# Performance work log

Hardware: AMD Instinct MI355X
Metric: run time of the kernel (lower is better)

Reference implementation:

```python
import jax, jax.numpy as jnp
import numpy as np

N_NODES = 50000
N_EDGES = 800000
D = 128


def gin_layer(x, edge_index, edge_attr, ee1, ee2, W1, b1, W2, b2):
    # PyG default flow source_to_target: x_j = x[edge_index[0]], aggregate at edge_index[1]
    src, dst = edge_index[0], edge_index[1]
    edge_emb = ee1[edge_attr[:, 0]] + ee2[edge_attr[:, 1]]           # [E, D]
    msg = x[src] + edge_emb                                          # [E, D]
    aggr = jax.ops.segment_sum(msg, dst, num_segments=x.shape[0])    # [N, D]
    h = jax.nn.relu(aggr @ W1 + b1)                                  # [N, 2D]
    return h @ W2 + b2                                               # [N, out]


def setup_inputs() -> dict:
    key = jax.random.key(0)
    ks = jax.random.split(key, 16)
    s = 1.0 / np.sqrt(D)
    inp = {
        "x": jax.random.normal(ks[0], (N_NODES, D), jnp.float32),
        "edge_index": jax.random.randint(ks[1], (2, N_EDGES), 0, N_NODES, dtype=jnp.int32),
        "edge_attr": jax.random.randint(ks[2], (N_EDGES, 2), 0, 3, dtype=jnp.int32),
        "ee1_0": jax.random.normal(ks[3], (6, D), jnp.float32) * s,
        "ee2_0": jax.random.normal(ks[4], (3, D), jnp.float32) * s,
        "W1_0": jax.random.normal(ks[5], (D, 2 * D), jnp.float32) * s,
        "b1_0": jnp.zeros((2 * D,), jnp.float32),
        "W2_0": jax.random.normal(ks[6], (2 * D, D), jnp.float32) * s,
        "b2_0": jnp.zeros((D,), jnp.float32),
        "ee1_1": jax.random.normal(ks[7], (6, D), jnp.float32) * s,
        "ee2_1": jax.random.normal(ks[8], (3, D), jnp.float32) * s,
        "W1_1": jax.random.normal(ks[9], (D, 2 * D), jnp.float32) * s,
        "b1_1": jnp.zeros((2 * D,), jnp.float32),
        "W2_1": jax.random.normal(ks[10], (2 * D, D), jnp.float32) * s,
        "b2_1": jnp.zeros((D,), jnp.float32),
    }
    return inp


def reference(x, edge_index, edge_attr, ee1_0, ee2_0, W1_0, b1_0, W2_0, b2_0,
              ee1_1, ee2_1, W1_1, b1_1, W2_1, b2_1):
    h = gin_layer(x, edge_index, edge_attr, ee1_0, ee2_0, W1_0, b1_0, W2_0, b2_0)
    h = jax.nn.relu(h)  # activation between GNN layers
    out = gin_layer(h, edge_index, edge_attr, ee1_1, ee2_1, W1_1, b1_1, W2_1, b2_1)
    return out  # jk='last'
```

## Files before the change

### kernel.cpp

```cpp
#include <hip/hip_runtime.h>

typedef __attribute__((ext_vector_type(8))) short s16x8;
typedef __attribute__((ext_vector_type(4))) float f32x4;
typedef unsigned short u16;
typedef unsigned char u8;
typedef unsigned long long u64;

#define D_FEAT 128
#define TILE1 4096

__device__ __forceinline__ u16 f2bf(float f) {
    unsigned u = __builtin_bit_cast(unsigned, f);
    u = u + 0x7fffu + ((u >> 16) & 1u);
    return (u16)(u >> 16);
}

__global__ __launch_bounds__(256) void tobf16_kernel(const float4* __restrict__ X,
                                                     u16* __restrict__ out, int n4) {
    int i = blockIdx.x * 256 + threadIdx.x;
    if (i < n4) {
        float4 v = X[i];
        uint2 p;
        p.x = (unsigned)f2bf(v.x) | ((unsigned)f2bf(v.y) << 16);
        p.y = (unsigned)f2bf(v.z) | ((unsigned)f2bf(v.w) << 16);
        *(uint2*)(out + (size_t)i * 4) = p;
    }
}

__global__ __launch_bounds__(256) void hist1_kernel(const int* __restrict__ dst,
                                                    int* __restrict__ ghist,
                                                    int E, int nb1, int bins) {
    __shared__ int h[256];
    const int t = threadIdx.x;
    h[t] = 0;
    __syncthreads();
    const int base = blockIdx.x * TILE1;
    #pragma unroll
    for (int j = 0; j < TILE1 / 256; ++j) {
        int e = base + j * 256 + t;
        if (e < E) atomicAdd(&h[dst[e] >> 8], 1);
    }
    __syncthreads();
    if (t < bins) ghist[t * nb1 + blockIdx.x] = h[t];
}

__global__ __launch_bounds__(256) void scan1a_kernel(int* __restrict__ ghist,
                                                     int* __restrict__ btot, int nb1) {
    __shared__ int wt[4];
    const int t = threadIdx.x, lane = t & 63, wid = t >> 6;
    const int bin = blockIdx.x;
    const int v = (t < nb1) ? ghist[bin * nb1 + t] : 0;
    int s = v;
    #pragma unroll
    for (int off = 1; off < 64; off <<= 1) {
        int u = __shfl_up(s, off, 64);
        if (lane >= off) s += u;
    }
    if (lane == 63) wt[wid] = s;
    __syncthreads();
    int add = 0;
    #pragma unroll
    for (int w = 0; w < 4; ++w) add += (w < wid) ? wt[w] : 0;
    s += add;
    if (t < nb1) ghist[bin * nb1 + t] = s - v;
    if (t == 255) btot[bin] = s;
}

__global__ __launch_bounds__(256) void scan1b_kernel(const int* __restrict__ btot,
                                                     int* __restrict__ bbase,
                                                     int* __restrict__ row_start, int bins) {
    __shared__ int wt[4];
    const int t = threadIdx.x, lane = t & 63, wid = t >> 6;
    const int v = (t < bins) ? btot[t] : 0;
    int s = v;
    #pragma unroll
    for (int off = 1; off < 64; off <<= 1) {
        int u = __shfl_up(s, off, 64);
        if (lane >= off) s += u;
    }
    if (lane == 63) wt[wid] = s;
    __syncthreads();
    int add = 0;
    #pragma unroll
    for (int w = 0; w < 4; ++w) add += (w < wid) ? wt[w] : 0;
    s += add;
    if (t < bins) bbase[t] = s - v;
    if (t == 255) bbase[bins] = s;
    if (t == 0) row_start[0] = 0;
}

__global__ __launch_bounds__(256) void scatter1_kernel(const int* __restrict__ src,
                                                       const int* __restrict__ dst,
                                                       const int* __restrict__ eattr,
                                                       const int* __restrict__ ghist,
                                                       const int* __restrict__ bbase,
                                                       u64* __restrict__ buf1,
                                                       int E, int nb1, int bins) {
    __shared__ int lofs[256];
    const int t = threadIdx.x;
    if (t < bins) lofs[t] = bbase[t] + ghist[t * nb1 + blockIdx.x];
    __syncthreads();
    const int base = blockIdx.x * TILE1;
    #pragma unroll
    for (int j = 0; j < TILE1 / 256; ++j) {
        int e = base + j * 256 + t;
        if (e < E) {
            int d = dst[e];
            int2 at = ((const int2*)eattr)[e];
            unsigned pay = (unsigned)src[e] | ((unsigned)(at.x * 3 + at.y) << 16);
            int pos = atomicAdd(&lofs[d >> 8], 1);
            buf1[pos] = ((u64)(unsigned)d << 32) | pay;
        }
    }
}

__global__ __launch_bounds__(256) void bucket2_kernel(const u64* __restrict__ buf1,
                                                      const int* __restrict__ bbase,
                                                      int* __restrict__ row_start,
                                                      unsigned* __restrict__ edges, int N) {
    __shared__ int cnt[256];
    __shared__ int cur[256];
    __shared__ int wt[4];
    const int t = threadIdx.x, lane = t & 63, wid = t >> 6;
    const int bin = blockIdx.x;
    const int lo = bbase[bin], hi = bbase[bin + 1];
    cnt[t] = 0;
    __syncthreads();
    for (int i = lo + t; i < hi; i += 256)
        atomicAdd(&cnt[(int)(buf1[i] >> 32) & 255], 1);
    __syncthreads();
    const int v = cnt[t];
    int s = v;
    #pragma unroll
    for (int off = 1; off < 64; off <<= 1) {
        int u = __shfl_up(s, off, 64);
        if (lane >= off) s += u;
    }
    if (lane == 63) wt[wid] = s;
    __syncthreads();
    int add = 0;
    #pragma unroll
    for (int w = 0; w < 4; ++w) add += (w < wid) ? wt[w] : 0;
    const int incl = s + add;
    const int g = bin * 256 + t;
    if (g < N) row_start[g + 1] = lo + incl;
    cur[t] = incl - v;
    __syncthreads();
    for (int i = lo + t; i < hi; i += 256) {
        u64 rec = buf1[i];
        int loc = atomicAdd(&cur[(int)(rec >> 32) & 255], 1);
        edges[lo + loc] = (unsigned)rec;
    }
}

__global__ __launch_bounds__(256) void transpose_kernel(const float* __restrict__ W1_0,
                                                        const float* __restrict__ W2_0,
                                                        const float* __restrict__ W1_1,
                                                        const float* __restrict__ W2_1,
                                                        u16* __restrict__ out) {
    int mat = blockIdx.y;
    const float* s = (mat == 0) ? W1_0 : (mat == 1) ? W2_0 : (mat == 2) ? W1_1 : W2_1;
    int K = (mat & 1) ? 256 : 128;
    int Nc = 384 - K;
    u16* d = out + mat * 32768;
    int idx = blockIdx.x * 256 + threadIdx.x;
    int n = idx / K, k = idx - n * K;
    d[idx] = f2bf(s[k * Nc + n]);
}

__global__ __launch_bounds__(128) void emb_kernel(const float* __restrict__ ee1_0,
                                                  const float* __restrict__ ee2_0,
                                                  const float* __restrict__ ee1_1,
                                                  const float* __restrict__ ee2_1,
                                                  float* __restrict__ emb) {
    int code = blockIdx.x;
    int layer = blockIdx.y;
    int d = threadIdx.x;
    int a0 = code / 3, a1 = code - a0 * 3;
    const float* e1 = layer ? ee1_1 : ee1_0;
    const float* e2 = layer ? ee2_1 : ee2_0;
    emb[layer * 18 * 128 + code * 128 + d] = e1[a0 * 128 + d] + e2[a1 * 128 + d];
}

__global__ __launch_bounds__(256) void aggregate_kernel(const u16* __restrict__ X,
                                                        const int* __restrict__ row_start,
                                                        const unsigned* __restrict__ edges,
                                                        const float* __restrict__ emb,
                                                        u16* __restrict__ A, int N) {
    __shared__ float semb[18 * 128];
    for (int i = threadIdx.x; i < 18 * 128; i += 256) semb[i] = emb[i];
    __syncthreads();
    const int node = blockIdx.x * 4 + (threadIdx.x >> 6);
    const int lane = threadIdx.x & 63;
    if (node >= N) return;
    int s = __builtin_amdgcn_readfirstlane(row_start[node]);
    const int e = __builtin_amdgcn_readfirstlane(row_start[node + 1]);
    const float2* sem2 = (const float2*)semb;
    float a0 = 0.f, a1 = 0.f;

    while (s < e) {
        const int take = (e - s < 64) ? (e - s) : 64;
        unsigned pl = edges[s + (lane < take ? lane : 0)];
        #pragma unroll
        for (int c = 0; c < 4; ++c) {
            const int cb = c * 16;
            if (cb < take) {
                unsigned ps[16];
                unsigned xv[16];
                float2 ev[16];
                #pragma unroll
                for (int j = 0; j < 16; ++j)
                    ps[j] = __builtin_amdgcn_readlane(pl, cb + j);
                #pragma unroll
                for (int j = 0; j < 16; ++j)
                    xv[j] = *(const unsigned*)(X + (ps[j] & 0xFFFFu) * D_FEAT + lane * 2);
                #pragma unroll
                for (int j = 0; j < 16; ++j)
                    ev[j] = sem2[(int)(ps[j] >> 16) * 64 + lane];
                #pragma unroll
                for (int j = 0; j < 16; ++j) {
                    const float m = (cb + j < take) ? 1.f : 0.f;
                    a0 += m * (__builtin_bit_cast(float, xv[j] << 16) + ev[j].x);
                    a1 += m * (__builtin_bit_cast(float, xv[j] & 0xFFFF0000u) + ev[j].y);
                }
            }
        }
        s += take;
    }
    unsigned outp = (unsigned)f2bf(a0) | ((unsigned)f2bf(a1) << 16);
    *(unsigned*)(A + node * D_FEAT + lane * 2) = outp;
}

#define HPAD 264
template <bool RELU2, bool OUTF32>
__global__ __launch_bounds__(256, 1) void mlp_kernel(const u16* __restrict__ A,
                                                     const u16* __restrict__ B1t,
                                                     const float* __restrict__ bias1,
                                                     const u16* __restrict__ B2t,
                                                     const float* __restrict__ bias2,
                                                     void* __restrict__ C, int M) {
    __shared__ __align__(16) u16 wbuf[32768];
    __shared__ __align__(16) u16 hh[4][16][HPAD];
    const int tid = threadIdx.x;
    const int wave = tid >> 6;
    const int lane = tid & 63;
    const int m16 = lane & 15;
    const int quad = lane >> 4;

    const int row0 = blockIdx.x * 64 + wave * 16;
    const int arow = row0 + m16;
    const bool avalid = arow < M;

    {
        const uint4* src = (const uint4*)B1t;
        #pragma unroll
        for (int i = 0; i < 16; ++i) {
            int s = i * 256 + tid;
            uint4 v = src[s];
            int c = (((s >> 8) * 4 + ((s >> 2) & 3)) << 6) | ((s & 3) << 4) | ((s >> 4) & 15);
            *(uint4*)(wbuf + c * 8) = v;
        }
    }

    s16x8 af[4];
    #pragma unroll
    for (int kb = 0; kb < 4; ++kb) af[kb] = s16x8{};
    if (avalid) {
        #pragma unroll
        for (int kb = 0; kb < 4; ++kb)
            af[kb] = *(const s16x8*)(A + arow * 128 + kb * 32 + quad * 8);
    }
    float b1v[16];
    #pragma unroll
    for (int t = 0; t < 16; ++t) b1v[t] = bias1[t * 16 + m16];

    __syncthreads();

    f32x4 acc[16];
    #pragma unroll
    for (int t = 0; t < 16; ++t) acc[t] = f32x4{0, 0, 0, 0};

    #pragma unroll
    for (int kb = 0; kb < 4; ++kb) {
        #pragma unroll
        for (int t = 0; t < 16; ++t) {
            s16x8 bf = *(const s16x8*)(wbuf + (((((t << 2) | kb) << 6) | lane) * 8));
            acc[t] = __builtin_amdgcn_mfma_f32_16x16x32_bf16(af[kb], bf, acc[t], 0, 0, 0);
        }
    }

    #pragma unroll
    for (int t = 0; t < 16; ++t) {
        const int col = t * 16 + m16;
        #pragma unroll
        for (int r = 0; r < 4; ++r) {
            float v = acc[t][r] + b1v[t];
            v = v > 0.f ? v : 0.f;
            hh[wave][quad * 4 + r][col] = f2bf(v);
        }
    }
    __syncthreads();

    {
        const uint4* src = (const uint4*)B2t;
        #pragma unroll
        for (int i = 0; i < 16; ++i) {
            int s = i * 256 + tid;
            uint4 v = src[s];
            int c = (((s >> 9) * 8 + ((s >> 2) & 7)) << 6) | ((s & 3) << 4) | ((s >> 5) & 15);
            *(uint4*)(wbuf + c * 8) = v;
        }
    }
    float b2v[8];
    #pragma unroll
    for (int t = 0; t < 8; ++t) b2v[t] = bias2[t * 16 + m16];

    __syncthreads();

    f32x4 acc2[8];
    #pragma unroll
    for (int t = 0; t < 8; ++t) acc2[t] = f32x4{0, 0, 0, 0};

    #pragma unroll
    for (int kb = 0; kb < 8; ++kb) {
        s16x8 haf = *(const s16x8*)(&hh[wave][m16][kb * 32 + quad * 8]);
        #pragma unroll
        for (int t = 0; t < 8; ++t) {
            s16x8 bf = *(const s16x8*)(wbuf + (((((t << 3) | kb) << 6) | lane) * 8));
            acc2[t] = __builtin_amdgcn_mfma_f32_16x16x32_bf16(haf, bf, acc2[t], 0, 0, 0);
        }
    }

    #pragma unroll
    for (int t = 0; t < 8; ++t) {
        const int col = t * 16 + m16;
        #pragma unroll
        for (int r = 0; r < 4; ++r) {
            const int row = row0 + quad * 4 + r;
            if (row < M) {
                float v = acc2[t][r] + b2v[t];
                if (RELU2) v = v > 0.f ? v : 0.f;
                if (OUTF32) ((float*)C)[row * 128 + col] = v;
                else        ((u16*)C)[row * 128 + col] = f2bf(v);
            }
        }
    }
}

extern "C" void kernel_launch(void* const* d_in, const int* in_sizes, int n_in,
                              void* d_out, int out_size, void* d_ws, size_t ws_size,
                              hipStream_t stream) {
    const int N = in_sizes[0] / D_FEAT;
    const int E = in_sizes[1] / 2;

    const float* x    = (const float*)d_in[0];
    const int* eidx   = (const int*)d_in[1];
    const int* eattr  = (const int*)d_in[2];
    const float* ee1_0 = (const float*)d_in[3];
    const float* ee2_0 = (const float*)d_in[4];
    const float* W1_0  = (const float*)d_in[5];
    const float* b1_0  = (const float*)d_in[6];
    const float* W2_0  = (const float*)d_in[7];
    const float* b2_0  = (const float*)d_in[8];
    const float* ee1_1 = (const float*)d_in[9];
    const float* ee2_1 = (const float*)d_in[10];
    const float* W1_1  = (const float*)d_in[11];
    const float* b1_1  = (const float*)d_in[12];
    const float* W2_1  = (const float*)d_in[13];
    const float* b2_1  = (const float*)d_in[14];

    const int nb1  = (E + TILE1 - 1) / TILE1;
    const int bins = (N + 255) / 256;

    char* ws = (char*)d_ws;
    size_t off = 0;
    auto alloc = [&](size_t bytes) { size_t o = off; off = (off + bytes + 255) & ~(size_t)255; return o; };
    size_t o_rowstart = alloc((size_t)(N + 1) * 4);
    size_t o_edges    = alloc((size_t)E * 4);
    size_t o_ghist    = alloc((size_t)bins * nb1 * 4);
    size_t o_base     = alloc((size_t)(bins + 1) * 4);
    size_t o_btot     = alloc((size_t)bins * 4);
    size_t o_emb      = alloc(2 * 18 * 128 * 4);
    size_t o_wt       = alloc(4 * 32768 * 2);
    size_t o_aa       = alloc((size_t)N * D_FEAT * 2);

    int*      row_start = (int*)(ws + o_rowstart);
    unsigned* edges     = (unsigned*)(ws + o_edges);
    int*      ghist     = (int*)(ws + o_ghist);
    int*      bbase     = (int*)(ws + o_base);
    int*      btot      = (int*)(ws + o_btot);
    float*    emb       = (float*)(ws + o_emb);
    u16*      W1t_0     = (u16*)(ws + o_wt);
    u16*      W2t_0     = W1t_0 + 32768;
    u16*      W1t_1     = W2t_0 + 32768;
    u16*      W2t_1     = W1t_1 + 32768;
    u16*      AA        = (u16*)(ws + o_aa);
    u64*      buf1      = (u64*)(ws + o_aa);

    u16* X2 = (u16*)d_out;
    u16* xb = (u16*)d_out + (size_t)N * D_FEAT;

    const int rows64 = (N + 63) / 64;
    const int aggB = (N + 3) / 4;
    const int n4 = N * D_FEAT / 4;

    tobf16_kernel<<<(n4 + 255) / 256, 256, 0, stream>>>((const float4*)x, xb, n4);

    hist1_kernel<<<nb1, 256, 0, stream>>>(eidx + E, ghist, E, nb1, bins);
    scan1a_kernel<<<bins, 256, 0, stream>>>(ghist, btot, nb1);
    scan1b_kernel<<<1, 256, 0, stream>>>(btot, bbase, row_start, bins);
    scatter1_kernel<<<nb1, 256, 0, stream>>>(eidx, eidx + E, eattr, ghist, bbase, buf1, E, nb1, bins);
    bucket2_kernel<<<bins, 256, 0, stream>>>(buf1, bbase, row_start, edges, N);

    emb_kernel<<<dim3(18, 2), 128, 0, stream>>>(ee1_0, ee2_0, ee1_1, ee2_1, emb);
    transpose_kernel<<<dim3(128, 4), 256, 0, stream>>>(W1_0, W2_0, W1_1, W2_1, W1t_0);

    aggregate_kernel<<<aggB, 256, 0, stream>>>(xb, row_start, edges, emb, AA, N);
    mlp_kernel<true, false><<<rows64, 256, 0, stream>>>(AA, W1t_0, b1_0, W2t_0, b2_0, X2, N);

    aggregate_kernel<<<aggB, 256, 0, stream>>>(X2, row_start, edges, emb + 18 * 128, AA, N);
    mlp_kernel<false, true><<<rows64, 256, 0, stream>>>(AA, W1t_1, b1_1, W2t_1, b2_1, d_out, N);
}
```

Before: 305.9 us.

## Make MLP kernel persistent with resident weights, swizzled LDS, and full-chunk aggregate path

The MLP kernel becomes persistent: 256 blocks each load both weight matrices into LDS once (160KB dynamic shared memory) and loop over row tiles, prefetching the next A tile while the current one computes. The hidden buffer uses an XOR swizzle instead of padding to avoid LDS bank conflicts. The aggregate kernel gains a fast path for full 16-edge chunks that skips the per-edge masking multiply. The aim is to stop reloading weights for every 64-row tile. The trade-offs are one block per CU with large LDS, fewer waves to hide latency, and an extra barrier per tile.

```diff
diff --git a/kernel.cpp b/kernel.cpp
--- a/kernel.cpp
+++ b/kernel.cpp
@@ -204,7 +204,25 @@
         #pragma unroll
         for (int c = 0; c < 4; ++c) {
             const int cb = c * 16;
-            if (cb < take) {
+            if (cb + 16 <= take) {
+                unsigned ps[16];
+                unsigned xv[16];
+                float2 ev[16];
+                #pragma unroll
+                for (int j = 0; j < 16; ++j)
+                    ps[j] = __builtin_amdgcn_readlane(pl, cb + j);
+                #pragma unroll
+                for (int j = 0; j < 16; ++j)
+                    xv[j] = *(const unsigned*)(X + (ps[j] & 0xFFFFu) * D_FEAT + lane * 2);
+                #pragma unroll
+                for (int j = 0; j < 16; ++j)
+                    ev[j] = sem2[(int)(ps[j] >> 16) * 64 + lane];
+                #pragma unroll
+                for (int j = 0; j < 16; ++j) {
+                    a0 += __builtin_bit_cast(float, xv[j] << 16) + ev[j].x;
+                    a1 += __builtin_bit_cast(float, xv[j] & 0xFFFF0000u) + ev[j].y;
+                }
+            } else if (cb < take) {
                 unsigned ps[16];
                 unsigned xv[16];
                 float2 ev[16];
@@ -231,119 +249,137 @@
     *(unsigned*)(A + node * D_FEAT + lane * 2) = outp;
 }
 
-#define HPAD 264
 template <bool RELU2, bool OUTF32>
 __global__ __launch_bounds__(256, 1) void mlp_kernel(const u16* __restrict__ A,
                                                      const u16* __restrict__ B1t,
                                                      const float* __restrict__ bias1,
                                                      const u16* __restrict__ B2t,
                                                      const float* __restrict__ bias2,
-                                                     void* __restrict__ C, int M) {
-    __shared__ __align__(16) u16 wbuf[32768];
-    __shared__ __align__(16) u16 hh[4][16][HPAD];
+                                                     void* __restrict__ C, int M, int nt) {
+    extern __shared__ __align__(16) u16 lds[];
+    u16* w1 = lds;
+    u16* w2 = lds + 32768;
+    u16* hh = lds + 65536;
     const int tid = threadIdx.x;
     const int wave = tid >> 6;
     const int lane = tid & 63;
     const int m16 = lane & 15;
     const int quad = lane >> 4;
 
-    const int row0 = blockIdx.x * 64 + wave * 16;
-    const int arow = row0 + m16;
-    const bool avalid = arow < M;
-
     {
-        const uint4* src = (const uint4*)B1t;
+        const uint4* src1 = (const uint4*)B1t;
+        const uint4* src2 = (const uint4*)B2t;
         #pragma unroll
         for (int i = 0; i < 16; ++i) {
             int s = i * 256 + tid;
-            uint4 v = src[s];
+            uint4 v = src1[s];
             int c = (((s >> 8) * 4 + ((s >> 2) & 3)) << 6) | ((s & 3) << 4) | ((s >> 4) & 15);
-            *(uint4*)(wbuf + c * 8) = v;
-        }
-    }
-
-    s16x8 af[4];
-    #pragma unroll
-    for (int kb = 0; kb < 4; ++kb) af[kb] = s16x8{};
-    if (avalid) {
-        #pragma unroll
-        for (int kb = 0; kb < 4; ++kb)
-            af[kb] = *(const s16x8*)(A + arow * 128 + kb * 32 + quad * 8);
-    }
-    float b1v[16];
-    #pragma unroll
-    for (int t = 0; t < 16; ++t) b1v[t] = bias1[t * 16 + m16];
-
-    __syncthreads();
-
-    f32x4 acc[16];
-    #pragma unroll
-    for (int t = 0; t < 16; ++t) acc[t] = f32x4{0, 0, 0, 0};
-
-    #pragma unroll
-    for (int kb = 0; kb < 4; ++kb) {
-        #pragma unroll
-        for (int t = 0; t < 16; ++t) {
-            s16x8 bf = *(const s16x8*)(wbuf + (((((t << 2) | kb) << 6) | lane) * 8));
-            acc[t] = __builtin_amdgcn_mfma_f32_16x16x32_bf16(af[kb], bf, acc[t], 0, 0, 0);
-        }
-    }
-
-    #pragma unroll
-    for (int t = 0; t < 16; ++t) {
-        const int col = t * 16 + m16;
-        #pragma unroll
-        for (int r = 0; r < 4; ++r) {
-            float v = acc[t][r] + b1v[t];
-            v = v > 0.f ? v : 0.f;
-            hh[wave][quad * 4 + r][col] = f2bf(v);
-        }
-    }
-    __syncthreads();
-
-    {
-        const uint4* src = (const uint4*)B2t;
+            *(uint4*)(w1 + c * 8) = v;
+        }
         #pragma unroll
         for (int i = 0; i < 16; ++i) {
             int s = i * 256 + tid;
-            uint4 v = src[s];
+            uint4 v = src2[s];
             int c = (((s >> 9) * 8 + ((s >> 2) & 7)) << 6) | ((s & 3) << 4) | ((s >> 5) & 15);
-            *(uint4*)(wbuf + c * 8) = v;
-        }
-    }
+            *(uint4*)(w2 + c * 8) = v;
+        }
+    }
+    float b1v[16];
+    #pragma unroll
+    for (int t = 0; t < 16; ++t) b1v[t] = bias1[t * 16 + m16];
     float b2v[8];
     #pragma unroll
     for (int t = 0; t < 8; ++t) b2v[t] = bias2[t * 16 + m16];
 
-    __syncthreads();
-
-    f32x4 acc2[8];
-    #pragma unroll
-    for (int t = 0; t < 8; ++t) acc2[t] = f32x4{0, 0, 0, 0};
-
-    #pragma unroll
-    for (int kb = 0; kb < 8; ++kb) {
-        s16x8 haf = *(const s16x8*)(&hh[wave][m16][kb * 32 + quad * 8]);
+    const int hbase = wave * 4096;
+
+    int tile = blockIdx.x;
+    s16x8 af[4];
+    #pragma unroll
+    for (int kb = 0; kb < 4; ++kb) af[kb] = s16x8{};
+    if (tile < nt) {
+        const int arow = tile * 64 + wave * 16 + m16;
+        if (arow < M) {
+            #pragma unroll
+            for (int kb = 0; kb < 4; ++kb)
+                af[kb] = *(const s16x8*)(A + (size_t)arow * 128 + kb * 32 + quad * 8);
+        }
+    }
+
+    __syncthreads();
+
+    for (; tile < nt; tile += 256) {
+        const int row0 = tile * 64 + wave * 16;
+
+        f32x4 acc[16];
+        #pragma unroll
+        for (int t = 0; t < 16; ++t) acc[t] = f32x4{0, 0, 0, 0};
+        #pragma unroll
+        for (int kb = 0; kb < 4; ++kb) {
+            #pragma unroll
+            for (int t = 0; t < 16; ++t) {
+                s16x8 bf = *(const s16x8*)(w1 + (((((t << 2) | kb) << 6) | lane) * 8));
+                acc[t] = __builtin_amdgcn_mfma_f32_16x16x32_bf16(af[kb], bf, acc[t], 0, 0, 0);
+            }
+        }
+
+        const int ntile = tile + 256;
+        s16x8 afn[4];
+        #pragma unroll
+        for (int kb = 0; kb < 4; ++kb) afn[kb] = s16x8{};
+        if (ntile < nt) {
+            const int arow = ntile * 64 + wave * 16 + m16;
+            if (arow < M) {
+                #pragma unroll
+                for (int kb = 0; kb < 4; ++kb)
+                    afn[kb] = *(const s16x8*)(A + (size_t)arow * 128 + kb * 32 + quad * 8);
+            }
+        }
+
+        #pragma unroll
+        for (int t = 0; t < 16; ++t) {
+            const int col = t * 16 + m16;
+            #pragma unroll
+            for (int r = 0; r < 4; ++r) {
+                const int row = quad * 4 + r;
+                float v = acc[t][r] + b1v[t];
+                v = v > 0.f ? v : 0.f;
+                hh[(hbase + row * 256 + col) ^ ((row & 7) << 3)] = f2bf(v);
+            }
+        }
+        __syncthreads();
+
+        f32x4 acc2[8];
+        #pragma unroll
+        for (int t = 0; t < 8; ++t) acc2[t] = f32x4{0, 0, 0, 0};
+        #pragma unroll
+        for (int kb = 0; kb < 8; ++kb) {
+            s16x8 haf = *(const s16x8*)(hh + ((hbase + m16 * 256 + kb * 32 + quad * 8) ^ ((m16 & 7) << 3)));
+            #pragma unroll
+            for (int t = 0; t < 8; ++t) {
+                s16x8 bf = *(const s16x8*)(w2 + (((((t << 3) | kb) << 6) | lane) * 8));
+                acc2[t] = __builtin_amdgcn_mfma_f32_16x16x32_bf16(haf, bf, acc2[t], 0, 0, 0);
+            }
+        }
+
         #pragma unroll
         for (int t = 0; t < 8; ++t) {
-            s16x8 bf = *(const s16x8*)(wbuf + (((((t << 3) | kb) << 6) | lane) * 8));
-            acc2[t] = __builtin_amdgcn_mfma_f32_16x16x32_bf16(haf, bf, acc2[t], 0, 0, 0);
-        }
-    }
-
-    #pragma unroll
-    for (int t = 0; t < 8; ++t) {
-        const int col = t * 16 + m16;
-        #pragma unroll
-        for (int r = 0; r < 4; ++r) {
-            const int row = row0 + quad * 4 + r;
-            if (row < M) {
-                float v = acc2[t][r] + b2v[t];
-                if (RELU2) v = v > 0.f ? v : 0.f;
-                if (OUTF32) ((float*)C)[row * 128 + col] = v;
-                else        ((u16*)C)[row * 128 + col] = f2bf(v);
-            }
-        }
+            const int col = t * 16 + m16;
+            #pragma unroll
+            for (int r = 0; r < 4; ++r) {
+                const int row = row0 + quad * 4 + r;
+                if (row < M) {
+                    float v = acc2[t][r] + b2v[t];
+                    if (RELU2) v = v > 0.f ? v : 0.f;
+                    if (OUTF32) ((float*)C)[(size_t)row * 128 + col] = v;
+                    else        ((u16*)C)[(size_t)row * 128 + col] = f2bf(v);
+                }
+            }
+        }
+        __syncthreads();
+
+        #pragma unroll
+        for (int kb = 0; kb < 4; ++kb) af[kb] = afn[kb];
     }
 }
 
@@ -400,9 +436,19 @@
     u16* X2 = (u16*)d_out;
     u16* xb = (u16*)d_out + (size_t)N * D_FEAT;
 
-    const int rows64 = (N + 63) / 64;
+    const int nt = (N + 63) / 64;
     const int aggB = (N + 3) / 4;
     const int n4 = N * D_FEAT / 4;
+    const int LDS_MLP = 163840;
+
+    static bool attr_done = false;
+    if (!attr_done) {
+        hipFuncSetAttribute((const void*)mlp_kernel<true, false>,
+                            hipFuncAttributeMaxDynamicSharedMemorySize, LDS_MLP);
+        hipFuncSetAttribute((const void*)mlp_kernel<false, true>,
+                            hipFuncAttributeMaxDynamicSharedMemorySize, LDS_MLP);
+        attr_done = true;
+    }
 
     tobf16_kernel<<<(n4 + 255) / 256, 256, 0, stream>>>((const float4*)x, xb, n4);
 
@@ -416,8 +462,8 @@
     transpose_kernel<<<dim3(128, 4), 256, 0, stream>>>(W1_0, W2_0, W1_1, W2_1, W1t_0);
 
     aggregate_kernel<<<aggB, 256, 0, stream>>>(xb, row_start, edges, emb, AA, N);
-    mlp_kernel<true, false><<<rows64, 256, 0, stream>>>(AA, W1t_0, b1_0, W2t_0, b2_0, X2, N);
+    mlp_kernel<true, false><<<256, 256, LDS_MLP, stream>>>(AA, W1t_0, b1_0, W2t_0, b2_0, X2, N, nt);
 
     aggregate_kernel<<<aggB, 256, 0, stream>>>(X2, row_start, edges, emb + 18 * 128, AA, N);
-    mlp_kernel<false, true><<<rows64, 256, 0, stream>>>(AA, W1t_1, b1_1, W2t_1, b2_1, d_out, N);
-}
+    mlp_kernel<false, true><<<256, 256, LDS_MLP, stream>>>(AA, W1t_1, b1_1, W2t_1, b2_1, d_out, N, nt);
+}
```

Measured after the change: 278.9 us. 1.1x faster.
